# Kernel optimization log

Hardware: AMD Instinct MI355X
Metric: run time of the kernel (lower is better)

## Reference

```python
import jax, jax.numpy as jnp
import numpy as np

B, S, HID = 1, 2048, 2048
H, D = 16, 128          # num heads, head_dim (H*D == HID)
L = 32                  # compression / selection block size
NB = S // L             # number of key blocks
NSEL = 8                # top-n selected blocks per query
WIN = 512               # sliding window size
SCALE = 1.0 / np.sqrt(D)
NEG = -1e9


def rotate_half(x):
    x1, x2 = x[..., : x.shape[-1] // 2], x[..., x.shape[-1] // 2 :]
    return jnp.concatenate([-x2, x1], axis=-1)


def rope_tables(dim, end, theta=10000.0):
    freqs = 1.0 / theta ** (jnp.arange(0, dim, 2, dtype=jnp.float32) / dim)
    ang = jnp.outer(jnp.arange(end, dtype=jnp.float32), freqs)  # [end, dim/2]
    cos = jnp.concatenate([jnp.cos(ang), jnp.cos(ang)], axis=-1)  # [end, dim]
    sin = jnp.concatenate([jnp.sin(ang), jnp.sin(ang)], axis=-1)
    return cos, sin


def setup_inputs() -> dict:
    key = jax.random.key(0)
    ks = jax.random.split(key, 10)
    std = 0.02
    return {
        "hidden_states": jax.random.normal(ks[0], (B, S, HID), jnp.float32),
        "Wq": jax.random.normal(ks[1], (HID, H * D), jnp.float32) * std,
        "bq": jnp.zeros((H * D,), jnp.float32),
        "Wk": jax.random.normal(ks[2], (HID, H * D), jnp.float32) * std,
        "bk": jnp.zeros((H * D,), jnp.float32),
        "Wv": jax.random.normal(ks[3], (HID, H * D), jnp.float32) * std,
        "bv": jnp.zeros((H * D,), jnp.float32),
        "Wg": jax.random.normal(ks[4], (H, D, 3), jnp.float32) * std,
        "bg": jnp.zeros((3,), jnp.float32),
    }


def _nsa_forward(hidden_states, Wq, bq, Wk, bk, Wv, bv, Wg, bg):
    # projections -> [B, H, S, D]
    def proj(W, b):
        return (hidden_states @ W + b).reshape(B, S, H, D).transpose(0, 2, 1, 3)

    q, k, v = proj(Wq, bq), proj(Wk, bk), proj(Wv, bv)

    cos, sin = rope_tables(D, S)  # [S, D]
    cos, sin = cos[None, None], sin[None, None]
    q = q * cos + rotate_half(q) * sin
    k = k * cos + rotate_half(k) * sin

    i = jnp.arange(S)
    t = jnp.arange(S)
    causal = t[None, :] <= i[:, None]  # [S, S]

    # ---- compressed branch: block mean-pooled K/V ----
    k_cmp = k.reshape(B, H, NB, L, D).mean(axis=3)  # [B,H,NB,D]
    v_cmp = v.reshape(B, H, NB, L, D).mean(axis=3)
    # block j visible if it ends at or before query position i
    blk_ok = ((jnp.arange(NB) + 1) * L - 1)[None, :] <= i[:, None]  # [S, NB]
    s_cmp = jnp.einsum("bhid,bhjd->bhij", q, k_cmp) * SCALE  # [B,H,S,NB]
    p_cmp = jax.nn.softmax(jnp.where(blk_ok[None, None], s_cmp, NEG), axis=-1)
    has_blk = blk_ok.any(axis=-1).astype(q.dtype)[None, None, :, None]  # [1,1,S,1]
    out_cmp = jnp.einsum("bhij,bhjd->bhid", p_cmp, v_cmp) * has_blk

    # ---- selection branch: top-n blocks from compressed scores ----
    idx = jax.lax.top_k(p_cmp, NSEL)[1]  # [B,H,S,NSEL]
    block_sel = (idx[..., None] == jnp.arange(NB)).any(axis=-2)  # [B,H,S,NB]
    cur_blk = (i[:, None] // L) == jnp.arange(NB)[None, :]  # always include own block
    block_sel = block_sel | cur_blk[None, None]
    tok_sel = jnp.take(block_sel, t // L, axis=-1)  # [B,H,S,S]
    mask_sel = tok_sel & causal[None, None]

    s = jnp.einsum("bhid,bhjd->bhij", q, k) * SCALE
    p_sel = jax.nn.softmax(jnp.where(mask_sel, s, NEG), axis=-1)
    out_sel = jnp.einsum("bhij,bhjd->bhid", p_sel, v)

    # ---- sliding-window branch ----
    mask_win = causal & ((i[:, None] - t[None, :]) < WIN)
    p_win = jax.nn.softmax(jnp.where(mask_win[None, None], s, NEG), axis=-1)
    out_win = jnp.einsum("bhij,bhjd->bhid", p_win, v)

    # ---- gated combine ----
    g = jax.nn.sigmoid(jnp.einsum("bhsd,hdg->bhsg", q, Wg) + bg)  # [B,H,S,3]
    out = (g[..., 0:1] * out_cmp + g[..., 1:2] * out_sel + g[..., 2:3] * out_win)
    return out.transpose(0, 2, 1, 3).reshape(B, S, H * D)


def reference(hidden_states, Wq, bq, Wk, bk, Wv, bv, Wg, bg):
    return _nsa_forward(hidden_states, Wq, bq, Wk, bk, Wv, bv, Wg, bg)
```

## Files before the change

### kernel.cpp

```cpp
#include <hip/hip_runtime.h>


#define SCALE_F 0.08838834764831845f
#define SCL2E   (0.08838834764831845f * 1.4426950408889634f)

typedef short  bf16x8 __attribute__((ext_vector_type(8)));
typedef short  s16x4  __attribute__((ext_vector_type(4)));
typedef float  f32x4  __attribute__((ext_vector_type(4)));

__device__ __forceinline__ unsigned short f2bfu(float x){
    unsigned u = __builtin_bit_cast(unsigned, x);
    u = (u + 0x7FFFu + ((u >> 16) & 1u)) >> 16;
    return (unsigned short)u;
}
__device__ __forceinline__ float bf2f(unsigned short b){
    unsigned u = ((unsigned)b) << 16;
    return __builtin_bit_cast(float, u);
}
__device__ __forceinline__ f32x4 mfma16(bf16x8 a, bf16x8 b, f32x4 c){
    return __builtin_amdgcn_mfma_f32_16x16x32_bf16(a, b, c, 0, 0, 0);
}

__global__ __launch_bounds__(64) void rope_table_k(float* __restrict__ ct,
                                                   float* __restrict__ st){
    int s = blockIdx.x, j = threadIdx.x;
    float fr  = 1.0f / powf(10000.0f, (float)j * (1.0f / 64.0f));
    float ang = (float)s * fr;
    ct[s * 64 + j] = cosf(ang);
    st[s * 64 + j] = sinf(ang);
}

template <bool LO>
__global__ __launch_bounds__(256) void prep_split(const float* __restrict__ src,
                                                  unsigned short* __restrict__ hi,
                                                  unsigned short* __restrict__ lo){
    size_t i = ((size_t)blockIdx.x * 256 + threadIdx.x) * 4;
    float4 x = *(const float4*)&src[i];
    unsigned short h0 = f2bfu(x.x), h1 = f2bfu(x.y), h2 = f2bfu(x.z), h3 = f2bfu(x.w);
    s16x4 hv; hv[0] = (short)h0; hv[1] = (short)h1; hv[2] = (short)h2; hv[3] = (short)h3;
    *(s16x4*)&hi[i] = hv;
    if (LO){
        s16x4 lv;
        lv[0] = (short)f2bfu(x.x - bf2f(h0)); lv[1] = (short)f2bfu(x.y - bf2f(h1));
        lv[2] = (short)f2bfu(x.z - bf2f(h2)); lv[3] = (short)f2bfu(x.w - bf2f(h3));
        *(s16x4*)&lo[i] = lv;
    }
}

__global__ __launch_bounds__(256) void prep_wT(const float* __restrict__ W,
                                               unsigned short* __restrict__ Th,
                                               unsigned short* __restrict__ Tl){
    __shared__ float T[64][65];
    const int k0 = blockIdx.x * 64, n0 = blockIdx.y * 64;
    const int tid = (int)threadIdx.x;
    #pragma unroll
    for (int it = 0; it < 16; ++it){
        int idx = tid + it * 256;
        int r = idx >> 6, c = idx & 63;
        T[c][r] = W[(size_t)(k0 + r) * 2048 + n0 + c];
    }
    __syncthreads();
    #pragma unroll
    for (int it = 0; it < 16; ++it){
        int idx = tid + it * 256;
        int n = idx >> 6, k = idx & 63;
        float v = T[n][k];
        unsigned short h = f2bfu(v);
        Th[(size_t)(n0 + n) * 2048 + k0 + k] = h;
        if (Tl) Tl[(size_t)(n0 + n) * 2048 + k0 + k] = f2bfu(v - bf2f(h));
    }
}

template <int P>
__global__ __launch_bounds__(256) void gemm_bf(
    const unsigned short* __restrict__ Ah, const unsigned short* __restrict__ Al,
    const unsigned short* __restrict__ Bh, const unsigned short* __restrict__ Bl,
    const float* __restrict__ bias,
    float* __restrict__ outF, unsigned short* __restrict__ outT)
{
    const unsigned short* Ap[2] = {Ah, Al};
    const unsigned short* Bp[2] = {Bh, Bl};
    const int m0  = blockIdx.x * 128;
    const int h   = blockIdx.y;
    const int tid = (int)threadIdx.x;
    const int l   = tid & 63, w = tid >> 6;
    const int wr  = w >> 1,  wc = w & 1;
    const int cc  = l & 15,  g  = l >> 4;

    __shared__ short As[P][128][40];
    __shared__ short Bs[P][128][40];

    f32x4 acc[4][4] = {};
    bf16x8 ra[P][2], rb[P][2];

    auto LOADSTEP = [&](int k0){
        #pragma unroll
        for (int p = 0; p < P; ++p)
            #pragma unroll
            for (int it = 0; it < 2; ++it){
                int c = tid + it * 256;
                int row = c >> 2, col8 = (c & 3) * 8;
                ra[p][it] = *(const bf16x8*)&Ap[p][(size_t)(m0 + row) * 2048 + k0 + col8];
                rb[p][it] = *(const bf16x8*)&Bp[p][(size_t)(h * 128 + row) * 2048 + k0 + col8];
            }
    };
    auto STORESTEP = [&](){
        #pragma unroll
        for (int p = 0; p < P; ++p)
            #pragma unroll
            for (int it = 0; it < 2; ++it){
                int c = tid + it * 256;
                int row = c >> 2, col8 = (c & 3) * 8;
                *(bf16x8*)&As[p][row][col8] = ra[p][it];
                *(bf16x8*)&Bs[p][row][col8] = rb[p][it];
            }
    };

    LOADSTEP(0); STORESTEP(); __syncthreads();
    for (int k0 = 0; k0 < 2048; k0 += 32){
        bool more = (k0 + 32) < 2048;
        if (more) LOADSTEP(k0 + 32);

        bf16x8 ah[4], bh[4];
        #pragma unroll
        for (int mt = 0; mt < 4; ++mt)
            ah[mt] = *(const bf16x8*)&As[0][wr * 64 + mt * 16 + cc][g * 8];
        #pragma unroll
        for (int nt = 0; nt < 4; ++nt)
            bh[nt] = *(const bf16x8*)&Bs[0][wc * 64 + nt * 16 + cc][g * 8];
        if (P == 2){
            bf16x8 al[4], bl[4];
            #pragma unroll
            for (int mt = 0; mt < 4; ++mt)
                al[mt] = *(const bf16x8*)&As[P - 1][wr * 64 + mt * 16 + cc][g * 8];
            #pragma unroll
            for (int nt = 0; nt < 4; ++nt)
                bl[nt] = *(const bf16x8*)&Bs[P - 1][wc * 64 + nt * 16 + cc][g * 8];
            #pragma unroll
            for (int mt = 0; mt < 4; ++mt)
                #pragma unroll
                for (int nt = 0; nt < 4; ++nt){
                    acc[mt][nt] = mfma16(ah[mt], bh[nt], acc[mt][nt]);
                    acc[mt][nt] = mfma16(ah[mt], bl[nt], acc[mt][nt]);
                    acc[mt][nt] = mfma16(al[mt], bh[nt], acc[mt][nt]);
                }
        } else {
            #pragma unroll
            for (int mt = 0; mt < 4; ++mt)
                #pragma unroll
                for (int nt = 0; nt < 4; ++nt)
                    acc[mt][nt] = mfma16(ah[mt], bh[nt], acc[mt][nt]);
        }
        __syncthreads();
        if (more){ STORESTEP(); __syncthreads(); }
    }

    #pragma unroll
    for (int mt = 0; mt < 4; ++mt)
        #pragma unroll
        for (int nt = 0; nt < 4; ++nt)
            #pragma unroll
            for (int j = 0; j < 4; ++j){
                int srow = m0 + wr * 64 + mt * 16 + g * 4 + j;
                int col  = wc * 64 + nt * 16 + cc;
                float v = acc[mt][nt][j] + bias[h * 128 + col];
                if (outF) outF[((size_t)h * 2048 + srow) * 128 + col] = v;
                else      outT[((size_t)h * 128 + col) * 2048 + srow] = f2bfu(v);
            }
}

__global__ __launch_bounds__(256) void rope_apply(
    float* __restrict__ qf, float* __restrict__ kf,
    const float* __restrict__ ct, const float* __restrict__ st)
{
    int idx = blockIdx.x * 256 + (int)threadIdx.x;
    int j = idx & 63;
    int s = (idx >> 6) & 2047;
    int h = (idx >> 17) & 15;
    int a = idx >> 21;
    float* p = (a ? kf : qf) + ((size_t)h * 2048 + s) * 128;
    float c = ct[s * 64 + j], sn = st[s * 64 + j];
    float x1 = p[j], x2 = p[j + 64];
    p[j]      = x1 * c - x2 * sn;
    p[j + 64] = x2 * c + x1 * sn;
}

__global__ __launch_bounds__(256) void cmp_mean(
    const float* __restrict__ kf, const unsigned short* __restrict__ vtbf,
    float* __restrict__ kcmp, float* __restrict__ vcmp)
{
    int idx = blockIdx.x * 256 + (int)threadIdx.x;
    int d  = idx & 127;
    int nb = (idx >> 7) & 63;
    int h  = idx >> 13;
    const float* kp = &kf[((size_t)h * 2048 + nb * 32) * 128 + d];
    float sk = 0.f;
    #pragma unroll
    for (int t = 0; t < 32; ++t) sk += kp[t * 128];
    const unsigned short* vp = &vtbf[((size_t)h * 128 + d) * 2048 + nb * 32];
    float sv = 0.f;
    #pragma unroll
    for (int t = 0; t < 32; ++t) sv += bf2f(vp[t]);
    kcmp[((size_t)h * 64 + nb) * 128 + d] = sk * 0.03125f;
    vcmp[((size_t)h * 64 + nb) * 128 + d] = sv * 0.03125f;
}

__global__ __launch_bounds__(256) void gates_k(
    const float* __restrict__ qf, const float* __restrict__ Wg,
    const float* __restrict__ bg, float* __restrict__ gout)
{
    int Gn = blockIdx.x * 256 + (int)threadIdx.x;
    int sub = Gn & 3, qh = Gn >> 2;
    if (sub == 3) return;
    int h = qh >> 11;
    const float* q  = &qf[(size_t)qh * 128];
    const float* wg = &Wg[(size_t)h * 384 + sub];
    float acc = 0.f;
    #pragma unroll 4
    for (int k = 0; k < 128; ++k) acc += q[k] * wg[k * 3];
    gout[(size_t)qh * 3 + sub] = 1.f / (1.f + expf(-(acc + bg[sub])));
}

__global__ __launch_bounds__(256) void cmp_attn(
    const float* __restrict__ qf, const float* __restrict__ kcmp,
    const float* __restrict__ vcmp, const float* __restrict__ gout,
    float* __restrict__ out, unsigned long long* __restrict__ bmask)
{
    const int h = blockIdx.y, qt = blockIdx.x, i0 = qt * 64;
    const int tid = (int)threadIdx.x;
    const int l = tid & 63, w = tid >> 6;
    const int ty = tid >> 4, tx = tid & 15;
    const int cc = l & 15, g = l >> 4;

    __shared__ __align__(16) char smem[65536];
    float4* qs4 = (float4*)smem;
    float4* kc4 = (float4*)(smem + 32768);
    unsigned short* vcT = (unsigned short*)smem;
    float* sc = (float*)(smem + 32768);
    unsigned short* ps = (unsigned short*)(smem + 32768 + 17408);

    #pragma unroll
    for (int it = 0; it < 8; ++it){
        int idx = tid + it * 256;
        int row = idx >> 5, c = idx & 31;
        int cs = c ^ ((row >> 2) & 7);
        qs4[row * 32 + cs] = *(const float4*)&qf[((size_t)h * 2048 + i0 + row) * 128 + c * 4];
        kc4[row * 32 + cs] = *(const float4*)&kcmp[((size_t)h * 64 + row) * 128 + c * 4];
    }
    __syncthreads();

    float acc[4][4] = {};
    #pragma unroll 2
    for (int k0 = 0; k0 < 32; ++k0){
        float4 qv[4], kv[4];
        #pragma unroll
        for (int j = 0; j < 4; ++j) qv[j] = qs4[(4 * ty + j) * 32 + (k0 ^ (ty & 7))];
        #pragma unroll
        for (int c = 0; c < 4; ++c) kv[c] = kc4[(4 * tx + c) * 32 + (k0 ^ (tx & 7))];
        #pragma unroll
        for (int j = 0; j < 4; ++j)
            #pragma unroll
            for (int c = 0; c < 4; ++c)
                acc[j][c] += qv[j].x * kv[c].x + qv[j].y * kv[c].y
                           + qv[j].z * kv[c].z + qv[j].w * kv[c].w;
    }
    __syncthreads();

    #pragma unroll
    for (int j = 0; j < 4; ++j){
        int r = 4 * ty + j, i = i0 + r;
        float4 sv;
        float* svp = (float*)&sv;
        #pragma unroll
        for (int c = 0; c < 4; ++c){
            int b = 4 * tx + c;
            svp[c] = (b * 32 + 31 <= i) ? acc[j][c] * SCALE_F : -1e9f;
        }
        *(float4*)&sc[r * 68 + 4 * tx] = sv;
    }
    #pragma unroll
    for (int it = 0; it < 8; ++it){
        int idx = tid + it * 256;
        int jb = idx >> 5, d4 = (idx & 31) * 4;
        float4 vx = *(const float4*)&vcmp[((size_t)h * 64 + jb) * 128 + d4];
        const float* vp = (const float*)&vx;
        #pragma unroll
        for (int jj = 0; jj < 4; ++jj)
            vcT[(d4 + jj) * 72 + jb] = f2bfu(vp[jj]);
    }
    __syncthreads();

    for (int qq = 0; qq < 16; ++qq){
        const int q = w * 16 + qq;
        float s = sc[q * 68 + l];
        float mx = s;
        #pragma unroll
        for (int off = 1; off < 64; off <<= 1) mx = fmaxf(mx, __shfl_xor(mx, off));
        float p = expf(s - mx);
        float sum = p;
        #pragma unroll
        for (int off = 1; off < 64; off <<= 1) sum += __shfl_xor(sum, off);
        p /= sum;
        ps[q * 72 + l] = f2bfu(p);

        unsigned long long sel = 1ULL << ((i0 + q) >> 5);
        unsigned long long key = (1ULL << 45) |
            ((unsigned long long)__builtin_bit_cast(unsigned, p) << 7) |
            (unsigned long long)(63 - l);
        #pragma unroll
        for (int it = 0; it < 8; ++it){
            unsigned long long k2 = key;
            #pragma unroll
            for (int off = 1; off < 64; off <<= 1){
                unsigned long long o = __shfl_xor(k2, off);
                k2 = (o > k2) ? o : k2;
            }
            int wb = 63 - (int)(k2 & 63ULL);
            sel |= 1ULL << wb;
            if (l == wb) key = 0ULL;
        }
        if (l == 0) bmask[(size_t)h * 2048 + i0 + q] = sel;
    }
    __syncthreads();

    f32x4 oacc[8] = {};
    #pragma unroll
    for (int kk = 0; kk < 2; ++kk){
        bf16x8 pa = *(const bf16x8*)&ps[(w * 16 + cc) * 72 + kk * 32 + g * 8];
        #pragma unroll
        for (int nt2 = 0; nt2 < 8; ++nt2){
            bf16x8 vfr = *(const bf16x8*)&vcT[(nt2 * 16 + cc) * 72 + kk * 32 + g * 8];
            oacc[nt2] = mfma16(pa, vfr, oacc[nt2]);
        }
    }
    #pragma unroll
    for (int j = 0; j < 4; ++j){
        int q = w * 16 + g * 4 + j, iq = i0 + q;
        float g0 = gout[((size_t)h * 2048 + iq) * 3];
        float f = (iq >= 31) ? g0 : 0.f;
        #pragma unroll
        for (int nt2 = 0; nt2 < 8; ++nt2)
            out[(size_t)iq * 2048 + h * 128 + nt2 * 16 + cc] = f * oacc[nt2][j];
    }
}

template <bool IS_SEL>
__global__ __launch_bounds__(256) void attn_main(
    const unsigned short* __restrict__ qbf,
    const unsigned short* __restrict__ kbf,
    const unsigned short* __restrict__ vtbf,
    const float* __restrict__ gates,
    const unsigned long long* __restrict__ bmask,
    float* __restrict__ out)
{
    const int h  = blockIdx.y;
    const int qt = IS_SEL ? 31 - (int)blockIdx.x : (int)blockIdx.x;
    const int i0 = qt * 64;
    const int tid = (int)threadIdx.x;
    const int l = tid & 63, w = tid >> 6;
    const int cc = l & 15,  g = l >> 4;

    __shared__ short Ks[64][136];
    __shared__ short Vt[128][72];
    __shared__ short Ps[4][16][72];

    unsigned long long um = 0;
    if (IS_SEL){
        um = bmask[(size_t)h * 2048 + i0 + l];
        #pragma unroll
        for (int off = 1; off < 64; off <<= 1) um |= __shfl_xor(um, off);
    }

    unsigned long long bm[4];
    int mrow[4];
    #pragma unroll
    for (int j = 0; j < 4; ++j){
        mrow[j] = i0 + w * 16 + g * 4 + j;
        bm[j] = IS_SEL ? bmask[(size_t)h * 2048 + mrow[j]] : 0ULL;
    }

    bf16x8 qfrag[4];
    {
        const unsigned short* qrow = &qbf[((size_t)h * 2048 + i0 + w * 16 + cc) * 128];
        #pragma unroll
        for (int kk = 0; kk < 4; ++kk)
            qfrag[kk] = *(const bf16x8*)&qrow[kk * 32 + g * 8];
    }

    f32x4 oacc[8] = {};
    float mrun[4], lrun[4];
    #pragma unroll
    for (int j = 0; j < 4; ++j){ mrun[j] = -1e30f; lrun[j] = 0.f; }

    const int chlo = IS_SEL ? 0 : (qt > 8 ? qt - 8 : 0);
    auto needed = [&](int ch)->bool {
        return IS_SEL ? (((um >> (2 * ch)) & 3ULL) != 0ULL) : true;
    };

    bf16x8 rk[4], rv[4];
    auto LOADC = [&](int ch){
        #pragma unroll
        for (int it = 0; it < 4; ++it){
            int c = tid + it * 256;
            rk[it] = *(const bf16x8*)&kbf[((size_t)h * 2048 + ch * 64 + (c >> 4)) * 128 + (c & 15) * 8];
            rv[it] = *(const bf16x8*)&vtbf[((size_t)h * 128 + (c >> 3)) * 2048 + ch * 64 + (c & 7) * 8];
        }
    };
    auto STOREC = [&](){
        #pragma unroll
        for (int it = 0; it < 4; ++it){
            int c = tid + it * 256;
            *(bf16x8*)&Ks[c >> 4][(c & 15) * 8] = rk[it];
            *(bf16x8*)&Vt[c >> 3][(c & 7) * 8] = rv[it];
        }
    };

    int cur = chlo;
    while (cur <= qt && !needed(cur)) ++cur;
    LOADC(cur); STOREC(); __syncthreads();

    while (cur <= qt){
        int nxt = cur + 1;
        while (nxt <= qt && !needed(nxt)) ++nxt;
        const bool more = (nxt <= qt);
        if (more) LOADC(nxt);

        f32x4 sacc[4] = {};
        #pragma unroll
        for (int kk = 0; kk < 4; ++kk)
            #pragma unroll
            for (int nt = 0; nt < 4; ++nt){
                bf16x8 kfr = *(const bf16x8*)&Ks[nt * 16 + cc][kk * 32 + g * 8];
                sacc[nt] = mfma16(qfrag[kk], kfr, sacc[nt]);
            }

        const int tbase = cur * 64;
        #pragma unroll
        for (int j = 0; j < 4; ++j){
            const int iq = mrow[j];
            float sj[4]; bool ok[4];
            float mx = -1e30f;
            #pragma unroll
            for (int nt = 0; nt < 4; ++nt){
                int t = tbase + nt * 16 + cc;
                bool o = (t <= iq) &&
                         (IS_SEL ? (((bm[j] >> (t >> 5)) & 1ULL) != 0ULL)
                                 : ((iq - t) < 512));
                float s = sacc[nt][j] * SCL2E;
                sj[nt] = s; ok[nt] = o;
                if (o) mx = fmaxf(mx, s);
            }
            #pragma unroll
            for (int off = 1; off < 16; off <<= 1)
                mx = fmaxf(mx, __shfl_xor(mx, off));
            float mnew = fmaxf(mrun[j], mx);
            float alpha = exp2f(mrun[j] - mnew);
            float psum = 0.f;
            #pragma unroll
            for (int nt = 0; nt < 4; ++nt){
                float p = ok[nt] ? exp2f(sj[nt] - mnew) : 0.f;
                psum += p;
                Ps[w][g * 4 + j][nt * 16 + cc] = (short)f2bfu(p);
            }
            #pragma unroll
            for (int off = 1; off < 16; off <<= 1)
                psum += __shfl_xor(psum, off);
            mrun[j] = mnew;
            lrun[j] = lrun[j] * alpha + psum;
            #pragma unroll
            for (int nt2 = 0; nt2 < 8; ++nt2) oacc[nt2][j] *= alpha;
        }
        __syncthreads();

        #pragma unroll
        for (int kk = 0; kk < 2; ++kk){
            bf16x8 pa = *(const bf16x8*)&Ps[w][cc][kk * 32 + g * 8];
            #pragma unroll
            for (int nt2 = 0; nt2 < 8; ++nt2){
                bf16x8 vfr = *(const bf16x8*)&Vt[nt2 * 16 + cc][kk * 32 + g * 8];
                oacc[nt2] = mfma16(pa, vfr, oacc[nt2]);
            }
        }
        __syncthreads();
        if (more){ STOREC(); __syncthreads(); }
        cur = more ? nxt : qt + 1;
    }

    const int GI = IS_SEL ? 1 : 2;
    #pragma unroll
    for (int j = 0; j < 4; ++j){
        const int iq = mrow[j];
        float gv  = gates[((size_t)h * 2048 + iq) * 3 + GI];
        float inv = gv / lrun[j];
        #pragma unroll
        for (int nt2 = 0; nt2 < 8; ++nt2){
            int d = nt2 * 16 + cc;
            out[(size_t)iq * 2048 + h * 128 + d] += oacc[nt2][j] * inv;
        }
    }
}

#define MB ((size_t)1 << 20)
#define OFF_QF   ((size_t)0)
#define OFF_KF   (16 * MB)
#define OFF_VT   (32 * MB)
#define OFF_XH   (40 * MB)
#define OFF_XL   (48 * MB)
#define OFF_WTH  (56 * MB)
#define OFF_WTL  (64 * MB)
#define OFF_COS  (72 * MB)
#define OFF_SIN  (72 * MB + 524288)
#define OFF_KC   (72 * MB + 1048576)
#define OFF_VC   (72 * MB + 1572864)
#define OFF_GATE (72 * MB + 2097152)
#define OFF_BM   (72 * MB + 2490368)

extern "C" void kernel_launch(void* const* d_in, const int* in_sizes, int n_in,
                              void* d_out, int out_size, void* d_ws, size_t ws_size,
                              hipStream_t stream)
{
    const float* X  = (const float*)d_in[0];
    const float* Wq = (const float*)d_in[1];
    const float* bq = (const float*)d_in[2];
    const float* Wk = (const float*)d_in[3];
    const float* bk = (const float*)d_in[4];
    const float* Wv = (const float*)d_in[5];
    const float* bv = (const float*)d_in[6];
    const float* Wg = (const float*)d_in[7];
    const float* bg = (const float*)d_in[8];
    float* out = (float*)d_out;

    char* ws = (char*)d_ws;
    float* qf   = (float*)(ws + OFF_QF);
    float* kf   = (float*)(ws + OFF_KF);
    unsigned short* vtbf = (unsigned short*)(ws + OFF_VT);
    unsigned short* Xh   = (unsigned short*)(ws + OFF_XH);
    unsigned short* Xl   = (unsigned short*)(ws + OFF_XL);
    unsigned short* WTh  = (unsigned short*)(ws + OFF_WTH);
    unsigned short* WTl  = (unsigned short*)(ws + OFF_WTL);
    unsigned short* qbf  = (unsigned short*)(ws + OFF_XH);
    unsigned short* kbf  = (unsigned short*)(ws + OFF_XL);
    float* cost  = (float*)(ws + OFF_COS);
    float* sint  = (float*)(ws + OFF_SIN);
    float* kcmp  = (float*)(ws + OFF_KC);
    float* vcmp  = (float*)(ws + OFF_VC);
    float* gatesb = (float*)(ws + OFF_GATE);
    unsigned long long* bmaskb = (unsigned long long*)(ws + OFF_BM);

    rope_table_k<<<2048, 64, 0, stream>>>(cost, sint);
    prep_split<true><<<4096, 256, 0, stream>>>(X, Xh, Xl);

    prep_wT<<<dim3(32, 32), 256, 0, stream>>>(Wq, WTh, WTl);
    gemm_bf<2><<<dim3(16, 16), 256, 0, stream>>>(Xh, Xl, WTh, WTl, bq, qf, nullptr);
    prep_wT<<<dim3(32, 32), 256, 0, stream>>>(Wk, WTh, WTl);
    gemm_bf<2><<<dim3(16, 16), 256, 0, stream>>>(Xh, Xl, WTh, WTl, bk, kf, nullptr);
    prep_wT<<<dim3(32, 32), 256, 0, stream>>>(Wv, WTh, nullptr);
    gemm_bf<1><<<dim3(16, 16), 256, 0, stream>>>(Xh, nullptr, WTh, nullptr, bv, nullptr, vtbf);

    rope_apply<<<16384, 256, 0, stream>>>(qf, kf, cost, sint);
    prep_split<false><<<4096, 256, 0, stream>>>(qf, qbf, nullptr);
    prep_split<false><<<4096, 256, 0, stream>>>(kf, kbf, nullptr);

    cmp_mean<<<512, 256, 0, stream>>>(kf, vtbf, kcmp, vcmp);
    gates_k<<<512, 256, 0, stream>>>(qf, Wg, bg, gatesb);
    cmp_attn<<<dim3(32, 16), 256, 0, stream>>>(qf, kcmp, vcmp, gatesb, out, bmaskb);

    attn_main<false><<<dim3(32, 16), 256, 0, stream>>>(qbf, kbf, vtbf, gatesb, bmaskb, out);
    attn_main<true><<<dim3(32, 16), 256, 0, stream>>>(qbf, kbf, vtbf, gatesb, bmaskb, out);
}
```

Baseline: 597.7 us.

## Fuse rope with bf16 cast, gates into cmp_attn, merge sel/win attention launches

```diff
diff --git a/kernel.cpp b/kernel.cpp
--- a/kernel.cpp
+++ b/kernel.cpp
@@ -30,7 +30,6 @@
     st[s * 64 + j] = sinf(ang);
 }
 
-template <bool LO>
 __global__ __launch_bounds__(256) void prep_split(const float* __restrict__ src,
                                                   unsigned short* __restrict__ hi,
                                                   unsigned short* __restrict__ lo){
@@ -39,12 +38,10 @@
     unsigned short h0 = f2bfu(x.x), h1 = f2bfu(x.y), h2 = f2bfu(x.z), h3 = f2bfu(x.w);
     s16x4 hv; hv[0] = (short)h0; hv[1] = (short)h1; hv[2] = (short)h2; hv[3] = (short)h3;
     *(s16x4*)&hi[i] = hv;
-    if (LO){
-        s16x4 lv;
-        lv[0] = (short)f2bfu(x.x - bf2f(h0)); lv[1] = (short)f2bfu(x.y - bf2f(h1));
-        lv[2] = (short)f2bfu(x.z - bf2f(h2)); lv[3] = (short)f2bfu(x.w - bf2f(h3));
-        *(s16x4*)&lo[i] = lv;
-    }
+    s16x4 lv;
+    lv[0] = (short)f2bfu(x.x - bf2f(h0)); lv[1] = (short)f2bfu(x.y - bf2f(h1));
+    lv[2] = (short)f2bfu(x.z - bf2f(h2)); lv[3] = (short)f2bfu(x.w - bf2f(h3));
+    *(s16x4*)&lo[i] = lv;
 }
 
 __global__ __launch_bounds__(256) void prep_wT(const float* __restrict__ W,
@@ -80,8 +77,12 @@
 {
     const unsigned short* Ap[2] = {Ah, Al};
     const unsigned short* Bp[2] = {Bh, Bl};
-    const int m0  = blockIdx.x * 128;
-    const int h   = blockIdx.y;
+
+    const int bid = (int)blockIdx.x;
+    const int xcd = bid & 7, idx = bid >> 3;
+    const int m0  = (((xcd >> 1) << 2) + (idx & 3)) * 128;
+    const int h   = ((xcd & 1) << 3) + (idx >> 2);
+
     const int tid = (int)threadIdx.x;
     const int l   = tid & 63, w = tid >> 6;
     const int wr  = w >> 1,  wc = w & 1;
@@ -171,6 +172,7 @@
 
 __global__ __launch_bounds__(256) void rope_apply(
     float* __restrict__ qf, float* __restrict__ kf,
+    unsigned short* __restrict__ qbb, unsigned short* __restrict__ kbb,
     const float* __restrict__ ct, const float* __restrict__ st)
 {
     int idx = blockIdx.x * 256 + (int)threadIdx.x;
@@ -178,11 +180,15 @@
     int s = (idx >> 6) & 2047;
     int h = (idx >> 17) & 15;
     int a = idx >> 21;
-    float* p = (a ? kf : qf) + ((size_t)h * 2048 + s) * 128;
+    size_t off = ((size_t)h * 2048 + s) * 128;
+    float* p = (a ? kf : qf) + off;
+    unsigned short* pb = (a ? kbb : qbb) + off;
     float c = ct[s * 64 + j], sn = st[s * 64 + j];
     float x1 = p[j], x2 = p[j + 64];
-    p[j]      = x1 * c - x2 * sn;
-    p[j + 64] = x2 * c + x1 * sn;
+    float y1 = x1 * c - x2 * sn;
+    float y2 = x2 * c + x1 * sn;
+    p[j]      = y1;  p[j + 64]  = y2;
+    pb[j] = f2bfu(y1); pb[j + 64] = f2bfu(y2);
 }
 
 __global__ __launch_bounds__(256) void cmp_mean(
@@ -205,26 +211,12 @@
     vcmp[((size_t)h * 64 + nb) * 128 + d] = sv * 0.03125f;
 }
 
-__global__ __launch_bounds__(256) void gates_k(
-    const float* __restrict__ qf, const float* __restrict__ Wg,
-    const float* __restrict__ bg, float* __restrict__ gout)
-{
-    int Gn = blockIdx.x * 256 + (int)threadIdx.x;
-    int sub = Gn & 3, qh = Gn >> 2;
-    if (sub == 3) return;
-    int h = qh >> 11;
-    const float* q  = &qf[(size_t)qh * 128];
-    const float* wg = &Wg[(size_t)h * 384 + sub];
-    float acc = 0.f;
-    #pragma unroll 4
-    for (int k = 0; k < 128; ++k) acc += q[k] * wg[k * 3];
-    gout[(size_t)qh * 3 + sub] = 1.f / (1.f + expf(-(acc + bg[sub])));
-}
-
 __global__ __launch_bounds__(256) void cmp_attn(
     const float* __restrict__ qf, const float* __restrict__ kcmp,
-    const float* __restrict__ vcmp, const float* __restrict__ gout,
-    float* __restrict__ out, unsigned long long* __restrict__ bmask)
+    const float* __restrict__ vcmp,
+    const float* __restrict__ Wg, const float* __restrict__ bg,
+    float* __restrict__ out, float* __restrict__ gout,
+    unsigned long long* __restrict__ bmask)
 {
     const int h = blockIdx.y, qt = blockIdx.x, i0 = qt * 64;
     const int tid = (int)threadIdx.x;
@@ -233,6 +225,7 @@
     const int cc = l & 15, g = l >> 4;
 
     __shared__ __align__(16) char smem[65536];
+    __shared__ float sgl[4][16][3];
     float4* qs4 = (float4*)smem;
     float4* kc4 = (float4*)(smem + 32768);
     unsigned short* vcT = (unsigned short*)smem;
@@ -249,6 +242,23 @@
     }
     __syncthreads();
 
+    {
+        int gi = l & 3, qq = l >> 2;
+        if (gi < 3){
+            int q = w * 16 + qq;
+            float acc = 0.f;
+            #pragma unroll
+            for (int c = 0; c < 32; ++c){
+                float4 qv = qs4[q * 32 + (c ^ ((q >> 2) & 7))];
+                const float* wgp = &Wg[(size_t)h * 384 + (c * 4) * 3 + gi];
+                acc += qv.x * wgp[0] + qv.y * wgp[3] + qv.z * wgp[6] + qv.w * wgp[9];
+            }
+            float gv = 1.f / (1.f + expf(-(acc + bg[gi])));
+            sgl[w][qq][gi] = gv;
+            gout[((size_t)h * 2048 + i0 + q) * 3 + gi] = gv;
+        }
+    }
+
     float acc[4][4] = {};
     #pragma unroll 2
     for (int k0 = 0; k0 < 32; ++k0){
@@ -336,7 +346,7 @@
     #pragma unroll
     for (int j = 0; j < 4; ++j){
         int q = w * 16 + g * 4 + j, iq = i0 + q;
-        float g0 = gout[((size_t)h * 2048 + iq) * 3];
+        float g0 = sgl[w][g * 4 + j][0];
         float f = (iq >= 31) ? g0 : 0.f;
         #pragma unroll
         for (int nt2 = 0; nt2 < 8; ++nt2)
@@ -344,8 +354,7 @@
     }
 }
 
-template <bool IS_SEL>
-__global__ __launch_bounds__(256) void attn_main(
+__global__ __launch_bounds__(256) void attn_ws(
     const unsigned short* __restrict__ qbf,
     const unsigned short* __restrict__ kbf,
     const unsigned short* __restrict__ vtbf,
@@ -354,7 +363,9 @@
     float* __restrict__ out)
 {
     const int h  = blockIdx.y;
-    const int qt = IS_SEL ? 31 - (int)blockIdx.x : (int)blockIdx.x;
+    const int bx = (int)blockIdx.x;
+    const bool SEL = bx < 32;
+    const int qt = SEL ? 31 - bx : 63 - bx;
     const int i0 = qt * 64;
     const int tid = (int)threadIdx.x;
     const int l = tid & 63, w = tid >> 6;
@@ -365,7 +376,7 @@
     __shared__ short Ps[4][16][72];
 
     unsigned long long um = 0;
-    if (IS_SEL){
+    if (SEL){
         um = bmask[(size_t)h * 2048 + i0 + l];
         #pragma unroll
         for (int off = 1; off < 64; off <<= 1) um |= __shfl_xor(um, off);
@@ -376,7 +387,7 @@
     #pragma unroll
     for (int j = 0; j < 4; ++j){
         mrow[j] = i0 + w * 16 + g * 4 + j;
-        bm[j] = IS_SEL ? bmask[(size_t)h * 2048 + mrow[j]] : 0ULL;
+        bm[j] = SEL ? bmask[(size_t)h * 2048 + mrow[j]] : 0ULL;
     }
 
     bf16x8 qfrag[4];
@@ -392,9 +403,9 @@
     #pragma unroll
     for (int j = 0; j < 4; ++j){ mrun[j] = -1e30f; lrun[j] = 0.f; }
 
-    const int chlo = IS_SEL ? 0 : (qt > 8 ? qt - 8 : 0);
+    const int chlo = SEL ? 0 : (qt > 8 ? qt - 8 : 0);
     auto needed = [&](int ch)->bool {
-        return IS_SEL ? (((um >> (2 * ch)) & 3ULL) != 0ULL) : true;
+        return SEL ? (((um >> (2 * ch)) & 3ULL) != 0ULL) : true;
     };
 
     bf16x8 rk[4], rv[4];
@@ -444,8 +455,8 @@
             for (int nt = 0; nt < 4; ++nt){
                 int t = tbase + nt * 16 + cc;
                 bool o = (t <= iq) &&
-                         (IS_SEL ? (((bm[j] >> (t >> 5)) & 1ULL) != 0ULL)
-                                 : ((iq - t) < 512));
+                         (SEL ? (((bm[j] >> (t >> 5)) & 1ULL) != 0ULL)
+                              : ((iq - t) < 512));
                 float s = sacc[nt][j] * SCL2E;
                 sj[nt] = s; ok[nt] = o;
                 if (o) mx = fmaxf(mx, s);
@@ -486,7 +497,7 @@
         cur = more ? nxt : qt + 1;
     }
 
-    const int GI = IS_SEL ? 1 : 2;
+    const int GI = SEL ? 1 : 2;
     #pragma unroll
     for (int j = 0; j < 4; ++j){
         const int iq = mrow[j];
@@ -495,25 +506,10 @@
         #pragma unroll
         for (int nt2 = 0; nt2 < 8; ++nt2){
             int d = nt2 * 16 + cc;
-            out[(size_t)iq * 2048 + h * 128 + d] += oacc[nt2][j] * inv;
-        }
-    }
-}
-
-#define MB ((size_t)1 << 20)
-#define OFF_QF   ((size_t)0)
-#define OFF_KF   (16 * MB)
-#define OFF_VT   (32 * MB)
-#define OFF_XH   (40 * MB)
-#define OFF_XL   (48 * MB)
-#define OFF_WTH  (56 * MB)
-#define OFF_WTL  (64 * MB)
-#define OFF_COS  (72 * MB)
-#define OFF_SIN  (72 * MB + 524288)
-#define OFF_KC   (72 * MB + 1048576)
-#define OFF_VC   (72 * MB + 1572864)
-#define OFF_GATE (72 * MB + 2097152)
-#define OFF_BM   (72 * MB + 2490368)
+            atomicAdd(&out[(size_t)iq * 2048 + h * 128 + d], oacc[nt2][j] * inv);
+        }
+    }
+}
 
 extern "C" void kernel_launch(void* const* d_in, const int* in_sizes, int n_in,
                               void* d_out, int out_size, void* d_ws, size_t ws_size,
@@ -530,41 +526,39 @@
     const float* bg = (const float*)d_in[8];
     float* out = (float*)d_out;
 
+    const size_t MBs = (size_t)1 << 20;
     char* ws = (char*)d_ws;
-    float* qf   = (float*)(ws + OFF_QF);
-    float* kf   = (float*)(ws + OFF_KF);
-    unsigned short* vtbf = (unsigned short*)(ws + OFF_VT);
-    unsigned short* Xh   = (unsigned short*)(ws + OFF_XH);
-    unsigned short* Xl   = (unsigned short*)(ws + OFF_XL);
-    unsigned short* WTh  = (unsigned short*)(ws + OFF_WTH);
-    unsigned short* WTl  = (unsigned short*)(ws + OFF_WTL);
-    unsigned short* qbf  = (unsigned short*)(ws + OFF_XH);
-    unsigned short* kbf  = (unsigned short*)(ws + OFF_XL);
-    float* cost  = (float*)(ws + OFF_COS);
-    float* sint  = (float*)(ws + OFF_SIN);
-    float* kcmp  = (float*)(ws + OFF_KC);
-    float* vcmp  = (float*)(ws + OFF_VC);
-    float* gatesb = (float*)(ws + OFF_GATE);
-    unsigned long long* bmaskb = (unsigned long long*)(ws + OFF_BM);
+
+    unsigned short* Xh  = (unsigned short*)(ws + 0 * MBs);
+    unsigned short* Xl  = (unsigned short*)(ws + 8 * MBs);
+    unsigned short* WTh = (unsigned short*)(ws + 16 * MBs);
+    unsigned short* WTl = (unsigned short*)(ws + 24 * MBs);
+    float* qf  = (float*)(ws + 32 * MBs);
+    float* kf  = (float*)(ws + 48 * MBs);
+    unsigned short* vtbf = (unsigned short*)(ws + 64 * MBs);
+    unsigned short* qbf  = (unsigned short*)(ws + 16 * MBs);
+    unsigned short* kbf  = (unsigned short*)(ws + 24 * MBs);
+    const size_t SM = 72 * MBs;
+    float* cost  = (float*)(ws + SM);
+    float* sint  = (float*)(ws + SM + 524288);
+    float* kcmp  = (float*)(ws + SM + 1048576);
+    float* vcmp  = (float*)(ws + SM + 1572864);
+    float* gatesb = (float*)(ws + SM + 2097152);
+    unsigned long long* bmaskb = (unsigned long long*)(ws + SM + 2490368);
 
     rope_table_k<<<2048, 64, 0, stream>>>(cost, sint);
-    prep_split<true><<<4096, 256, 0, stream>>>(X, Xh, Xl);
+    prep_split<<<4096, 256, 0, stream>>>(X, Xh, Xl);
 
     prep_wT<<<dim3(32, 32), 256, 0, stream>>>(Wq, WTh, WTl);
-    gemm_bf<2><<<dim3(16, 16), 256, 0, stream>>>(Xh, Xl, WTh, WTl, bq, qf, nullptr);
+    gemm_bf<2><<<256, 256, 0, stream>>>(Xh, Xl, WTh, WTl, bq, qf, nullptr);
     prep_wT<<<dim3(32, 32), 256, 0, stream>>>(Wk, WTh, WTl);
-    gemm_bf<2><<<dim3(16, 16), 256, 0, stream>>>(Xh, Xl, WTh, WTl, bk, kf, nullptr);
+    gemm_bf<2><<<256, 256, 0, stream>>>(Xh, Xl, WTh, WTl, bk, kf, nullptr);
     prep_wT<<<dim3(32, 32), 256, 0, stream>>>(Wv, WTh, nullptr);
-    gemm_bf<1><<<dim3(16, 16), 256, 0, stream>>>(Xh, nullptr, WTh, nullptr, bv, nullptr, vtbf);
-
-    rope_apply<<<16384, 256, 0, stream>>>(qf, kf, cost, sint);
-    prep_split<false><<<4096, 256, 0, stream>>>(qf, qbf, nullptr);
-    prep_split<false><<<4096, 256, 0, stream>>>(kf, kbf, nullptr);
-
+    gemm_bf<1><<<256, 256, 0, stream>>>(Xh, nullptr, WTh, nullptr, bv, nullptr, vtbf);
+
+    rope_apply<<<16384, 256, 0, stream>>>(qf, kf, qbf, kbf, cost, sint);
     cmp_mean<<<512, 256, 0, stream>>>(kf, vtbf, kcmp, vcmp);
-    gates_k<<<512, 256, 0, stream>>>(qf, Wg, bg, gatesb);
-    cmp_attn<<<dim3(32, 16), 256, 0, stream>>>(qf, kcmp, vcmp, gatesb, out, bmaskb);
-
-    attn_main<false><<<dim3(32, 16), 256, 0, stream>>>(qbf, kbf, vtbf, gatesb, bmaskb, out);
-    attn_main<true><<<dim3(32, 16), 256, 0, stream>>>(qbf, kbf, vtbf, gatesb, bmaskb, out);
-}
+    cmp_attn<<<dim3(32, 16), 256, 0, stream>>>(qf, kcmp, vcmp, Wg, bg,
+                                               out, gatesb, bmaskb);
+    attn_ws<<<dim3(64, 16), 256, 0, stream>>>(qbf, kbf, vtbf, gatesb, bmaskb, out);
+}
```

After: 667.6 us. 11.7% more time.
